# Optimization experiments

Measured on AMD Instinct MI355X. Metric: run time of the kernel, lower is better.

## Reference

```python
import jax, jax.numpy as jnp
import numpy as np
import math

B, S, E, NH = 1024, 16, 32, 4  # batch, seq, attn embed dim, heads
H = 64                          # lstm1 hidden; lstm2 hidden = H//2 = E


def _pos_encoding(s, d):
    pos = jnp.arange(s, dtype=jnp.float32)[:, None]
    div = jnp.exp(jnp.arange(0, d, 2, dtype=jnp.float32) * (-math.log(10000.0) / d))
    pe = jnp.zeros((s, d), jnp.float32)
    pe = pe.at[:, 0::2].set(jnp.sin(pos * div))
    pe = pe.at[:, 1::2].set(jnp.cos(pos * div))
    return pe


def _lstm(x, wih, whh, bih, bhh):
    # x: [B,S,in]; PyTorch gate order i,f,g,o; h0=c0=0
    b = x.shape[0]
    h_dim = whh.shape[1]
    xg = jnp.einsum('bsi,gi->bsg', x, wih) + bih + bhh  # precompute input contribution

    def step(carry, xt):
        h, c = carry
        g = xt + h @ whh.T
        i, f, gg, o = jnp.split(g, 4, axis=-1)
        c = jax.nn.sigmoid(f) * c + jax.nn.sigmoid(i) * jnp.tanh(gg)
        h = jax.nn.sigmoid(o) * jnp.tanh(c)
        return (h, c), h

    h0 = jnp.zeros((b, h_dim), x.dtype)
    _, hs = jax.lax.scan(step, (h0, h0), jnp.swapaxes(xg, 0, 1))
    return jnp.swapaxes(hs, 0, 1)  # [B,S,H]


def setup_inputs() -> dict:
    key = jax.random.key(0)
    ks = jax.random.split(key, 24)

    def rn(k, shape, s=0.15):
        return jax.random.normal(k, shape, jnp.float32) * s

    return {
        'x': jax.random.normal(ks[0], (B, S, 1), jnp.float32),
        'emb_w': rn(ks[1], (32, 1)), 'emb_b': rn(ks[2], (32,), 0.05),
        'l1_wih': rn(ks[3], (4 * H, 32)), 'l1_whh': rn(ks[4], (4 * H, H)),
        'l1_bih': rn(ks[5], (4 * H,), 0.05), 'l1_bhh': rn(ks[6], (4 * H,), 0.05),
        'l2_wih': rn(ks[7], (4 * (H // 2), H)), 'l2_whh': rn(ks[8], (4 * (H // 2), H // 2)),
        'l2_bih': rn(ks[9], (4 * (H // 2),), 0.05), 'l2_bhh': rn(ks[10], (4 * (H // 2),), 0.05),
        'attn_w': rn(ks[11], (3 * E, E)), 'attn_b': rn(ks[12], (3 * E,), 0.05),
        'attn_ow': rn(ks[13], (E, E)), 'attn_ob': rn(ks[14], (E,), 0.05),
        'd1_w': rn(ks[15], (64, E)), 'd1_b': rn(ks[16], (64,), 0.05),
        'bn1_g': jnp.ones((64,), jnp.float32), 'bn1_b': jnp.zeros((64,), jnp.float32),
        'd2_w': rn(ks[17], (32, 64)), 'd2_b': rn(ks[18], (32,), 0.05),
        'bn2_g': jnp.ones((32,), jnp.float32), 'bn2_b': jnp.zeros((32,), jnp.float32),
        'd3_w': rn(ks[19], (1, 32)), 'd3_b': rn(ks[20], (1,), 0.05),
    }


def reference(x, emb_w, emb_b, l1_wih, l1_whh, l1_bih, l1_bhh,
              l2_wih, l2_whh, l2_bih, l2_bhh,
              attn_w, attn_b, attn_ow, attn_ob,
              d1_w, d1_b, bn1_g, bn1_b, d2_w, d2_b, bn2_g, bn2_b, d3_w, d3_b):
    eps = 1e-5
    h = x @ emb_w.T + emb_b                      # [B,S,32]
    h = h + _pos_encoding(h.shape[1], h.shape[2])
    l1 = _lstm(h, l1_wih, l1_whh, l1_bih, l1_bhh)          # [B,S,64]  (dropout: eval -> id)
    l2 = _lstm(l1, l2_wih, l2_whh, l2_bih, l2_bhh)         # [B,S,32]
    l2 = l2 + l1[:, :, :l2.shape[2]]                        # residual

    # nn.MultiheadAttention with default batch_first=False: attends over axis 0 (=B here),
    # faithful to the original module's behavior.
    L, N, _ = l2.shape
    hd = E // NH
    qkv = l2 @ attn_w.T + attn_b
    q, k, v = jnp.split(qkv, 3, axis=-1)
    q = q.reshape(L, N, NH, hd) * (1.0 / math.sqrt(hd))
    k = k.reshape(L, N, NH, hd)
    v = v.reshape(L, N, NH, hd)
    scores = jnp.einsum('lnhd,mnhd->nhlm', q, k)           # [S,4,B,B]
    a = jax.nn.softmax(scores, axis=-1)
    att = jnp.einsum('nhlm,mnhd->lnhd', a, v).reshape(L, N, E)
    att = att @ attn_ow.T + attn_ob

    z = att[:, -1, :]                                       # [B,32]

    def bn(t, g, b):  # eval-mode BatchNorm1d with fresh running stats (mean=0, var=1)
        return t * (g / jnp.sqrt(1.0 + eps)) + b

    z = jax.nn.relu(bn(z @ d1_w.T + d1_b, bn1_g, bn1_b))
    z = jax.nn.relu(bn(z @ d2_w.T + d2_b, bn2_g, bn2_b))
    return jax.nn.sigmoid(z @ d3_w.T + d3_b)                # [B,1]
```

## Files before the change

### kernel.cpp

```cpp
#include <hip/hip_runtime.h>
#include <math.h>


__device__ __forceinline__ float sigf(float x) { return 1.0f / (1.0f + __expf(-x)); }
__device__ __forceinline__ float tanh_f(float x) {
    float a = fabsf(x);
    float e = __expf(2.0f * a);
    float t = 1.0f - 2.0f / (e + 1.0f);
    return copysignf(t, x);
}

__global__ void prep_kernel(const float* __restrict__ emb_w, const float* __restrict__ emb_b,
                            const float* __restrict__ wih1, const float* __restrict__ bih1,
                            const float* __restrict__ bhh1,
                            float* __restrict__ A1, float* __restrict__ C1) {
    int s = blockIdx.x, t = threadIdx.x;
    float c = bih1[t] + bhh1[t];
#pragma unroll
    for (int i = 0; i < 32; i++) {
        int j = (i >> 1) * 2;
        float div = __expf(-0.28782313662425574f * (float)j);
        float ang = (float)s * div;
        float pe = (i & 1) ? __cosf(ang) : __sinf(ang);
        c += (emb_b[i] + pe) * wih1[t * 32 + i];
    }
    C1[s * 256 + t] = c;
    if (s == 0) {
        float a = 0.f;
#pragma unroll
        for (int i = 0; i < 32; i++) a += emb_w[i] * wih1[t * 32 + i];
        A1[t] = a;
    }
}

__global__ __launch_bounds__(256, 2) void lstm_kernel(
    const float* __restrict__ x,
    const float* __restrict__ whh1,
    const float* __restrict__ wih2,
    const float* __restrict__ whh2,
    const float* __restrict__ bih2, const float* __restrict__ bhh2,
    const float* __restrict__ attn_w, const float* __restrict__ attn_b,
    const float* __restrict__ A1, const float* __restrict__ C1,
    float* __restrict__ Q, float* __restrict__ K, float* __restrict__ V) {
    int t = threadIdx.x;
    int base = blockIdx.x * 2;
    __shared__ __align__(16) float h1s[2][2][64];
    __shared__ __align__(16) float h2s[2][2][32];
    __shared__ __align__(16) float g1s[2][256];
    __shared__ __align__(16) float g2p[2][2][128];
    __shared__ __align__(16) float l2l[2][32];
    __shared__ float xs[2][16];

    float w1[64];
#pragma unroll
    for (int k = 0; k < 64; k++) w1[k] = whh1[t * 64 + k];
    int g = t & 127, half = t >> 7;
    float w2a[32];
#pragma unroll
    for (int k = 0; k < 32; k++) w2a[k] = wih2[g * 64 + half * 32 + k];
    float w2b[16];
#pragma unroll
    for (int k = 0; k < 16; k++) w2b[k] = whh2[g * 32 + half * 16 + k];
    float A1t = A1[t];
    float C1r[16];
#pragma unroll
    for (int s = 0; s < 16; s++) C1r[s] = C1[s * 256 + t];
    int j2 = t & 31;
    float bi2 = bih2[j2] + bhh2[j2];
    float bf2 = bih2[32 + j2] + bhh2[32 + j2];
    float bg2 = bih2[64 + j2] + bhh2[64 + j2];
    float bo2 = bih2[96 + j2] + bhh2[96 + j2];

    if (t < 128) h1s[0][t >> 6][t & 63] = 0.f;
    if (t < 64) h2s[0][t >> 5][t & 31] = 0.f;
    if (t < 32) xs[t >> 4][t & 15] = x[(base + (t >> 4)) * 16 + (t & 15)];
    float c1 = 0.f, c2 = 0.f;
    __syncthreads();

#pragma unroll
    for (int s = 0; s < 16; s++) {
        const int p = s & 1, pn = p ^ 1;
        {
            const float4* h0 = (const float4*)h1s[p][0];
            const float4* h1 = (const float4*)h1s[p][1];
            float a0 = xs[0][s] * A1t + C1r[s];
            float a1 = xs[1][s] * A1t + C1r[s];
#pragma unroll
            for (int k4 = 0; k4 < 16; k4++) {
                float4 u = h0[k4];
                float4 v = h1[k4];
                a0 += u.x * w1[4 * k4] + u.y * w1[4 * k4 + 1] + u.z * w1[4 * k4 + 2] + u.w * w1[4 * k4 + 3];
                a1 += v.x * w1[4 * k4] + v.y * w1[4 * k4 + 1] + v.z * w1[4 * k4 + 2] + v.w * w1[4 * k4 + 3];
            }
            g1s[0][t] = a0;
            g1s[1][t] = a1;
        }
        __syncthreads();
        if (t < 128) {
            int b = t >> 6, j = t & 63;
            float gi = g1s[b][j], gf = g1s[b][64 + j], gg = g1s[b][128 + j], go = g1s[b][192 + j];
            c1 = sigf(gf) * c1 + sigf(gi) * tanh_f(gg);
            h1s[pn][b][j] = sigf(go) * tanh_f(c1);
        }
        __syncthreads();
        {
#pragma unroll
            for (int b = 0; b < 2; b++) {
                const float4* hn = (const float4*)(&h1s[pn][b][half * 32]);
                const float4* ho = (const float4*)(&h2s[p][b][half * 16]);
                float d0 = 0.f, d1 = 0.f;
#pragma unroll
                for (int k4 = 0; k4 < 8; k4++) {
                    float4 u = hn[k4];
                    d0 += u.x * w2a[4 * k4] + u.y * w2a[4 * k4 + 1] + u.z * w2a[4 * k4 + 2] + u.w * w2a[4 * k4 + 3];
                }
#pragma unroll
                for (int k4 = 0; k4 < 4; k4++) {
                    float4 u = ho[k4];
                    d1 += u.x * w2b[4 * k4] + u.y * w2b[4 * k4 + 1] + u.z * w2b[4 * k4 + 2] + u.w * w2b[4 * k4 + 3];
                }
                g2p[b][half][g] = d0 + d1;
            }
        }
        __syncthreads();
        if (t < 64) {
            int b = t >> 5, j = t & 31;
            float gi = g2p[b][0][j] + g2p[b][1][j] + bi2;
            float gf = g2p[b][0][32 + j] + g2p[b][1][32 + j] + bf2;
            float gg = g2p[b][0][64 + j] + g2p[b][1][64 + j] + bg2;
            float go = g2p[b][0][96 + j] + g2p[b][1][96 + j] + bo2;
            c2 = sigf(gf) * c2 + sigf(gi) * tanh_f(gg);
            h2s[pn][b][j] = sigf(go) * tanh_f(c2);
        }
    }

    __syncthreads();
    if (t < 64) {
        int b = t >> 5, j = t & 31;
        l2l[b][j] = h2s[0][b][j] + h1s[0][b][j];
    }
    __syncthreads();
    if (t < 192) {
        int b = (t >= 96), r = t - b * 96;
        const float4* lw = (const float4*)l2l[b];
        const float4* aw = (const float4*)(attn_w + r * 32);
        float acc = attn_b[r];
#pragma unroll
        for (int k4 = 0; k4 < 8; k4++) {
            float4 u = lw[k4], w = aw[k4];
            acc += u.x * w.x + u.y * w.y + u.z * w.z + u.w * w.w;
        }
        int gb = base + b;
        if (r < 32) Q[gb * 32 + r] = acc * 0.35355339059327373f;
        else if (r < 64) K[gb * 32 + (r - 32)] = acc;
        else V[gb * 32 + (r - 64)] = acc;
    }
}

__global__ __launch_bounds__(256, 2) void attn_kernel(
    const float* __restrict__ Q, const float* __restrict__ K, const float* __restrict__ V,
    float* __restrict__ pm, float* __restrict__ ps, float* __restrict__ pacc) {
    int c = blockIdx.x & 15, lt = blockIdx.x >> 4;
    int t = threadIdx.x;
    int h = t >> 6, l = lt * 64 + (t & 63);
    __shared__ __align__(16) float Ks[64 * 32];
    __shared__ __align__(16) float Vs[64 * 32];
    {
        const float4* Kg = (const float4*)(K + c * 2048);
        const float4* Vg = (const float4*)(V + c * 2048);
        float4* K4 = (float4*)Ks;
        float4* V4 = (float4*)Vs;
        K4[t] = Kg[t];
        K4[t + 256] = Kg[t + 256];
        V4[t] = Vg[t];
        V4[t + 256] = Vg[t + 256];
    }
    const float4* qg = (const float4*)(Q + l * 32 + h * 8);
    float4 q0 = qg[0], q1 = qg[1];
    __syncthreads();
    float m_r = -1e30f, l_r = 0.f;
    float4 acc0 = {0, 0, 0, 0}, acc1 = {0, 0, 0, 0};
#pragma unroll 4
    for (int m = 0; m < 64; m++) {
        const float4* k4 = (const float4*)(Ks + m * 32 + h * 8);
        float4 ka = k4[0], kb = k4[1];
        float s = q0.x * ka.x + q0.y * ka.y + q0.z * ka.z + q0.w * ka.w +
                  q1.x * kb.x + q1.y * kb.y + q1.z * kb.z + q1.w * kb.w;
        const float4* v4 = (const float4*)(Vs + m * 32 + h * 8);
        float4 va = v4[0], vb = v4[1];
        float nm = fmaxf(m_r, s);
        float f = __expf(m_r - nm);
        float pp = __expf(s - nm);
        l_r = l_r * f + pp;
        acc0.x = acc0.x * f + pp * va.x;
        acc0.y = acc0.y * f + pp * va.y;
        acc0.z = acc0.z * f + pp * va.z;
        acc0.w = acc0.w * f + pp * va.w;
        acc1.x = acc1.x * f + pp * vb.x;
        acc1.y = acc1.y * f + pp * vb.y;
        acc1.z = acc1.z * f + pp * vb.z;
        acc1.w = acc1.w * f + pp * vb.w;
        m_r = nm;
    }
    int idx = (c * 4 + h) * 1024 + l;
    pm[idx] = m_r;
    ps[idx] = l_r;
    float4* po = (float4*)(pacc + idx * 8);
    po[0] = acc0;
    po[1] = acc1;
}

__global__ __launch_bounds__(256) void head_kernel(
    const float* __restrict__ pm, const float* __restrict__ ps, const float* __restrict__ pacc,
    const float* __restrict__ ow, const float* __restrict__ ob,
    const float* __restrict__ d1w, const float* __restrict__ d1b,
    const float* __restrict__ g1, const float* __restrict__ b1,
    const float* __restrict__ d2w, const float* __restrict__ d2b,
    const float* __restrict__ g2, const float* __restrict__ b2,
    const float* __restrict__ d3w, const float* __restrict__ d3b,
    float* __restrict__ out) {
    int wid = threadIdx.x >> 6, j = threadIdx.x & 63;
    int l = blockIdx.x * 4 + wid;
    __shared__ float att_s[4][32], z_s[4][32], r1s[4][64];
    if (j < 32) {
        int h = j >> 3, d = j & 7;
        float M = -1e30f;
#pragma unroll
        for (int c = 0; c < 16; c++) M = fmaxf(M, pm[(c * 4 + h) * 1024 + l]);
        float den = 0.f, num = 0.f;
#pragma unroll
        for (int c = 0; c < 16; c++) {
            int idx = (c * 4 + h) * 1024 + l;
            float e = __expf(pm[idx] - M);
            den += e * ps[idx];
            num += e * pacc[idx * 8 + d];
        }
        att_s[wid][j] = num / den;
    }
    __syncthreads();
    if (j < 32) {
        float a = ob[j];
#pragma unroll
        for (int i = 0; i < 32; i++) a += att_s[wid][i] * ow[j * 32 + i];
        z_s[wid][j] = a;
    }
    __syncthreads();
    const float inv = rsqrtf(1.0f + 1e-5f);
    if (j < 64) {
        float a = d1b[j];
#pragma unroll
        for (int i = 0; i < 32; i++) a += z_s[wid][i] * d1w[j * 32 + i];
        a = a * (g1[j] * inv) + b1[j];
        r1s[wid][j] = fmaxf(a, 0.f);
    }
    __syncthreads();
    if (j < 32) {
        float a = d2b[j];
#pragma unroll
        for (int i = 0; i < 64; i++) a += r1s[wid][i] * d2w[j * 64 + i];
        a = a * (g2[j] * inv) + b2[j];
        float r2 = fmaxf(a, 0.f);
        float p = r2 * d3w[j];
        p += __shfl_down(p, 16);
        p += __shfl_down(p, 8);
        p += __shfl_down(p, 4);
        p += __shfl_down(p, 2);
        p += __shfl_down(p, 1);
        if (j == 0) out[l] = 1.0f / (1.0f + __expf(-(p + d3b[0])));
    }
}

extern "C" void kernel_launch(void* const* d_in, const int* in_sizes, int n_in,
                              void* d_out, int out_size, void* d_ws, size_t ws_size,
                              hipStream_t stream) {
    const float* x      = (const float*)d_in[0];
    const float* emb_w  = (const float*)d_in[1];
    const float* emb_b  = (const float*)d_in[2];
    const float* l1_wih = (const float*)d_in[3];
    const float* l1_whh = (const float*)d_in[4];
    const float* l1_bih = (const float*)d_in[5];
    const float* l1_bhh = (const float*)d_in[6];
    const float* l2_wih = (const float*)d_in[7];
    const float* l2_whh = (const float*)d_in[8];
    const float* l2_bih = (const float*)d_in[9];
    const float* l2_bhh = (const float*)d_in[10];
    const float* attn_w = (const float*)d_in[11];
    const float* attn_b = (const float*)d_in[12];
    const float* attn_ow = (const float*)d_in[13];
    const float* attn_ob = (const float*)d_in[14];
    const float* d1_w  = (const float*)d_in[15];
    const float* d1_b  = (const float*)d_in[16];
    const float* bn1_g = (const float*)d_in[17];
    const float* bn1_b = (const float*)d_in[18];
    const float* d2_w  = (const float*)d_in[19];
    const float* d2_b  = (const float*)d_in[20];
    const float* bn2_g = (const float*)d_in[21];
    const float* bn2_b = (const float*)d_in[22];
    const float* d3_w  = (const float*)d_in[23];
    const float* d3_b  = (const float*)d_in[24];
    float* out = (float*)d_out;

    float* ws   = (float*)d_ws;
    float* A1   = ws;
    float* C1   = ws + 256;
    float* Q    = ws + 4352;
    float* K    = ws + 37120;
    float* V    = ws + 69888;
    float* pm   = ws + 102656;
    float* ps   = ws + 168192;
    float* pacc = ws + 233728;

    prep_kernel<<<16, 256, 0, stream>>>(emb_w, emb_b, l1_wih, l1_bih, l1_bhh, A1, C1);
    lstm_kernel<<<512, 256, 0, stream>>>(x, l1_whh, l2_wih, l2_whh, l2_bih, l2_bhh,
                                         attn_w, attn_b, A1, C1, Q, K, V);
    attn_kernel<<<256, 256, 0, stream>>>(Q, K, V, pm, ps, pacc);
    head_kernel<<<256, 256, 0, stream>>>(pm, ps, pacc, attn_ow, attn_ob, d1_w, d1_b,
                                         bn1_g, bn1_b, d2_w, d2_b, bn2_g, bn2_b,
                                         d3_w, d3_b, out);
}
```

Baseline: 159.6 us.

## Run both LSTM recurrences on bf16 MFMA with 16 sequences per block

The LSTM kernel now processes 16 batch rows per block with bf16 16x16x32 MFMA instructions, replacing the per-thread fp32 dot products. Weights are packed into registers as bf16 fragments, and hidden states go to XOR-swizzled LDS. The embedding plus positional-encoding input projection is folded into the MFMA as an extra K-slice, which removes the separate prep kernel. The grid drops from 512 to 64 blocks, trading parallelism for far fewer instructions per step, and bf16 rounding of weights and states adds precision risk.

```diff
diff --git a/kernel.cpp b/kernel.cpp
--- a/kernel.cpp
+++ b/kernel.cpp
@@ -1,6 +1,9 @@
 #include <hip/hip_runtime.h>
 #include <math.h>
 
+
+typedef __attribute__((ext_vector_type(8))) short short8v;
+typedef __attribute__((ext_vector_type(4))) float f32x4;
 
 __device__ __forceinline__ float sigf(float x) { return 1.0f / (1.0f + __expf(-x)); }
 __device__ __forceinline__ float tanh_f(float x) {
@@ -9,151 +12,210 @@
     float t = 1.0f - 2.0f / (e + 1.0f);
     return copysignf(t, x);
 }
-
-__global__ void prep_kernel(const float* __restrict__ emb_w, const float* __restrict__ emb_b,
-                            const float* __restrict__ wih1, const float* __restrict__ bih1,
-                            const float* __restrict__ bhh1,
-                            float* __restrict__ A1, float* __restrict__ C1) {
-    int s = blockIdx.x, t = threadIdx.x;
-    float c = bih1[t] + bhh1[t];
-#pragma unroll
-    for (int i = 0; i < 32; i++) {
-        int j = (i >> 1) * 2;
-        float div = __expf(-0.28782313662425574f * (float)j);
-        float ang = (float)s * div;
-        float pe = (i & 1) ? __cosf(ang) : __sinf(ang);
-        c += (emb_b[i] + pe) * wih1[t * 32 + i];
-    }
-    C1[s * 256 + t] = c;
-    if (s == 0) {
-        float a = 0.f;
-#pragma unroll
-        for (int i = 0; i < 32; i++) a += emb_w[i] * wih1[t * 32 + i];
-        A1[t] = a;
-    }
-}
-
-__global__ __launch_bounds__(256, 2) void lstm_kernel(
+__device__ __forceinline__ unsigned short f2bf(float f) {
+    unsigned int u = __float_as_uint(f);
+    unsigned int r = (u + 0x7FFFu + ((u >> 16) & 1u)) >> 16;
+    return (unsigned short)r;
+}
+
+__global__ __launch_bounds__(256, 1) void lstm_kernel(
     const float* __restrict__ x,
-    const float* __restrict__ whh1,
-    const float* __restrict__ wih2,
-    const float* __restrict__ whh2,
+    const float* __restrict__ emb_w, const float* __restrict__ emb_b,
+    const float* __restrict__ wih1, const float* __restrict__ whh1,
+    const float* __restrict__ bih1, const float* __restrict__ bhh1,
+    const float* __restrict__ wih2, const float* __restrict__ whh2,
     const float* __restrict__ bih2, const float* __restrict__ bhh2,
     const float* __restrict__ attn_w, const float* __restrict__ attn_b,
-    const float* __restrict__ A1, const float* __restrict__ C1,
     float* __restrict__ Q, float* __restrict__ K, float* __restrict__ V) {
-    int t = threadIdx.x;
-    int base = blockIdx.x * 2;
-    __shared__ __align__(16) float h1s[2][2][64];
-    __shared__ __align__(16) float h2s[2][2][32];
-    __shared__ __align__(16) float g1s[2][256];
-    __shared__ __align__(16) float g2p[2][2][128];
-    __shared__ __align__(16) float l2l[2][32];
-    __shared__ float xs[2][16];
-
-    float w1[64];
-#pragma unroll
-    for (int k = 0; k < 64; k++) w1[k] = whh1[t * 64 + k];
-    int g = t & 127, half = t >> 7;
-    float w2a[32];
-#pragma unroll
-    for (int k = 0; k < 32; k++) w2a[k] = wih2[g * 64 + half * 32 + k];
-    float w2b[16];
-#pragma unroll
-    for (int k = 0; k < 16; k++) w2b[k] = whh2[g * 32 + half * 16 + k];
-    float A1t = A1[t];
-    float C1r[16];
-#pragma unroll
-    for (int s = 0; s < 16; s++) C1r[s] = C1[s * 256 + t];
-    int j2 = t & 31;
-    float bi2 = bih2[j2] + bhh2[j2];
-    float bf2 = bih2[32 + j2] + bhh2[32 + j2];
-    float bg2 = bih2[64 + j2] + bhh2[64 + j2];
-    float bo2 = bih2[96 + j2] + bhh2[96 + j2];
-
-    if (t < 128) h1s[0][t >> 6][t & 63] = 0.f;
-    if (t < 64) h2s[0][t >> 5][t & 31] = 0.f;
-    if (t < 32) xs[t >> 4][t & 15] = x[(base + (t >> 4)) * 16 + (t & 15)];
-    float c1 = 0.f, c2 = 0.f;
-    __syncthreads();
+    const int tid = threadIdx.x;
+    const int w = tid >> 6, lane = tid & 63;
+    const int l15 = lane & 15, q4 = lane >> 4;
+    const int base = blockIdx.x * 16;
+
+    __shared__ __align__(16) unsigned char E_raw[16 * 1024];
+    __shared__ __align__(16) unsigned char H1_raw[2][2048];
+    __shared__ __align__(16) unsigned char H2_raw[2][1024];
+    __shared__ __align__(16) float L1F[16][64];
+    __shared__ __align__(16) float L2F[16][32];
+
+    const unsigned jx7 = (unsigned)(l15 & 7) << 4;
+    const unsigned jx4 = (unsigned)(l15 & 3) << 4;
+
+    short8v w1f[4][3];
+#pragma unroll
+    for (int t = 0; t < 4; t++) {
+        const int row = (w + 4 * t) * 16 + l15;
+#pragma unroll
+        for (int sl = 0; sl < 3; sl++) {
+            short8v f;
+#pragma unroll
+            for (int e = 0; e < 8; e++) {
+                int k = sl * 32 + q4 * 8 + e;
+                float v = (k < 64) ? whh1[row * 64 + k] : wih1[row * 32 + (k - 64)];
+                f[e] = (short)f2bf(v);
+            }
+            w1f[t][sl] = f;
+        }
+    }
+    float b1r[4][4];
+#pragma unroll
+    for (int t = 0; t < 4; t++)
+#pragma unroll
+        for (int e = 0; e < 4; e++) {
+            int r = (w + 4 * t) * 16 + q4 * 4 + e;
+            b1r[t][e] = bih1[r] + bhh1[r];
+        }
+
+    short8v w2f[4][3];
+    float b2r[4][4];
+    if (w < 2) {
+#pragma unroll
+        for (int t = 0; t < 4; t++) {
+            const int row = (w + 2 * t) * 16 + l15;
+#pragma unroll
+            for (int sl = 0; sl < 3; sl++) {
+                short8v f;
+#pragma unroll
+                for (int e = 0; e < 8; e++) {
+                    int k = sl * 32 + q4 * 8 + e;
+                    float v = (k < 64) ? wih2[row * 64 + k] : whh2[row * 32 + (k - 64)];
+                    f[e] = (short)f2bf(v);
+                }
+                w2f[t][sl] = f;
+            }
+#pragma unroll
+            for (int e = 0; e < 4; e++) {
+                int r = (w + 2 * t) * 16 + q4 * 4 + e;
+                b2r[t][e] = bih2[r] + bhh2[r];
+            }
+        }
+    }
+
+    *(unsigned long long*)(H1_raw[0] + tid * 8) = 0ULL;
+    if (tid < 128) *(unsigned long long*)(H2_raw[0] + tid * 8) = 0ULL;
+    {
+        const int je = tid >> 4, se = tid & 15;
+        float xv = x[(base + je) * 16 + se];
+        float ev[32];
+#pragma unroll
+        for (int ii = 0; ii < 16; ii++) {
+            float d = __expf(-0.28782313662425574f * (float)(2 * ii));
+            float ang = (float)se * d;
+            ev[2 * ii] = xv * emb_w[2 * ii] + emb_b[2 * ii] + __sinf(ang);
+            ev[2 * ii + 1] = xv * emb_w[2 * ii + 1] + emb_b[2 * ii + 1] + __cosf(ang);
+        }
+        unsigned jm = (unsigned)(je & 3) << 4;
+#pragma unroll
+        for (int b = 0; b < 4; b++) {
+            short8v pk;
+#pragma unroll
+            for (int e = 0; e < 8; e++) pk[e] = (short)f2bf(ev[b * 8 + e]);
+            *(short8v*)(&E_raw[se * 1024 + je * 64 + (((unsigned)(b * 16)) ^ jm)]) = pk;
+        }
+    }
+    float c1[4] = {0.f, 0.f, 0.f, 0.f};
+    float c2[4] = {0.f, 0.f, 0.f, 0.f};
+    __syncthreads();
+
+    const int u0 = w * 16 + q4 * 4;
+    const int u20 = w * 16 + q4 * 4;
 
 #pragma unroll
     for (int s = 0; s < 16; s++) {
         const int p = s & 1, pn = p ^ 1;
+        const unsigned char* H1p = H1_raw[p];
+        unsigned char* H1n = H1_raw[pn];
+        short8v B0 = *(const short8v*)(H1p + (((unsigned)(l15 * 128 + q4 * 16)) ^ jx7));
+        short8v B1 = *(const short8v*)(H1p + (((unsigned)(l15 * 128 + 64 + q4 * 16)) ^ jx7));
+        short8v BE = *(const short8v*)(&E_raw[s * 1024] + (((unsigned)(l15 * 64 + q4 * 16)) ^ jx4));
+        f32x4 a0 = {b1r[0][0], b1r[0][1], b1r[0][2], b1r[0][3]};
+        f32x4 a1 = {b1r[1][0], b1r[1][1], b1r[1][2], b1r[1][3]};
+        f32x4 a2 = {b1r[2][0], b1r[2][1], b1r[2][2], b1r[2][3]};
+        f32x4 a3 = {b1r[3][0], b1r[3][1], b1r[3][2], b1r[3][3]};
+        a0 = __builtin_amdgcn_mfma_f32_16x16x32_bf16(w1f[0][0], B0, a0, 0, 0, 0);
+        a1 = __builtin_amdgcn_mfma_f32_16x16x32_bf16(w1f[1][0], B0, a1, 0, 0, 0);
+        a2 = __builtin_amdgcn_mfma_f32_16x16x32_bf16(w1f[2][0], B0, a2, 0, 0, 0);
+        a3 = __builtin_amdgcn_mfma_f32_16x16x32_bf16(w1f[3][0], B0, a3, 0, 0, 0);
+        a0 = __builtin_amdgcn_mfma_f32_16x16x32_bf16(w1f[0][1], B1, a0, 0, 0, 0);
+        a1 = __builtin_amdgcn_mfma_f32_16x16x32_bf16(w1f[1][1], B1, a1, 0, 0, 0);
+        a2 = __builtin_amdgcn_mfma_f32_16x16x32_bf16(w1f[2][1], B1, a2, 0, 0, 0);
+        a3 = __builtin_amdgcn_mfma_f32_16x16x32_bf16(w1f[3][1], B1, a3, 0, 0, 0);
+        a0 = __builtin_amdgcn_mfma_f32_16x16x32_bf16(w1f[0][2], BE, a0, 0, 0, 0);
+        a1 = __builtin_amdgcn_mfma_f32_16x16x32_bf16(w1f[1][2], BE, a1, 0, 0, 0);
+        a2 = __builtin_amdgcn_mfma_f32_16x16x32_bf16(w1f[2][2], BE, a2, 0, 0, 0);
+        a3 = __builtin_amdgcn_mfma_f32_16x16x32_bf16(w1f[3][2], BE, a3, 0, 0, 0);
+        float h1v[4];
+#pragma unroll
+        for (int e = 0; e < 4; e++) {
+            c1[e] = sigf(a1[e]) * c1[e] + sigf(a0[e]) * tanh_f(a2[e]);
+            h1v[e] = sigf(a3[e]) * tanh_f(c1[e]);
+        }
         {
-            const float4* h0 = (const float4*)h1s[p][0];
-            const float4* h1 = (const float4*)h1s[p][1];
-            float a0 = xs[0][s] * A1t + C1r[s];
-            float a1 = xs[1][s] * A1t + C1r[s];
-#pragma unroll
-            for (int k4 = 0; k4 < 16; k4++) {
-                float4 u = h0[k4];
-                float4 v = h1[k4];
-                a0 += u.x * w1[4 * k4] + u.y * w1[4 * k4 + 1] + u.z * w1[4 * k4 + 2] + u.w * w1[4 * k4 + 3];
-                a1 += v.x * w1[4 * k4] + v.y * w1[4 * k4 + 1] + v.z * w1[4 * k4 + 2] + v.w * w1[4 * k4 + 3];
-            }
-            g1s[0][t] = a0;
-            g1s[1][t] = a1;
-        }
+            unsigned long long pk =
+                (unsigned long long)f2bf(h1v[0]) | ((unsigned long long)f2bf(h1v[1]) << 16) |
+                ((unsigned long long)f2bf(h1v[2]) << 32) | ((unsigned long long)f2bf(h1v[3]) << 48);
+            *(unsigned long long*)(H1n + (((unsigned)(l15 * 128 + u0 * 2)) ^ jx7)) = pk;
+        }
+        if (s == 15) *(float4*)(&L1F[l15][u0]) = make_float4(h1v[0], h1v[1], h1v[2], h1v[3]);
         __syncthreads();
-        if (t < 128) {
-            int b = t >> 6, j = t & 63;
-            float gi = g1s[b][j], gf = g1s[b][64 + j], gg = g1s[b][128 + j], go = g1s[b][192 + j];
-            c1 = sigf(gf) * c1 + sigf(gi) * tanh_f(gg);
-            h1s[pn][b][j] = sigf(go) * tanh_f(c1);
+        if (w < 2) {
+            const unsigned char* H2p = H2_raw[p];
+            short8v C0 = *(const short8v*)(H1n + (((unsigned)(l15 * 128 + q4 * 16)) ^ jx7));
+            short8v C1f = *(const short8v*)(H1n + (((unsigned)(l15 * 128 + 64 + q4 * 16)) ^ jx7));
+            short8v C2 = *(const short8v*)(H2p + (((unsigned)(l15 * 64 + q4 * 16)) ^ jx4));
+            f32x4 d0 = {b2r[0][0], b2r[0][1], b2r[0][2], b2r[0][3]};
+            f32x4 d1 = {b2r[1][0], b2r[1][1], b2r[1][2], b2r[1][3]};
+            f32x4 d2 = {b2r[2][0], b2r[2][1], b2r[2][2], b2r[2][3]};
+            f32x4 d3 = {b2r[3][0], b2r[3][1], b2r[3][2], b2r[3][3]};
+            d0 = __builtin_amdgcn_mfma_f32_16x16x32_bf16(w2f[0][0], C0, d0, 0, 0, 0);
+            d1 = __builtin_amdgcn_mfma_f32_16x16x32_bf16(w2f[1][0], C0, d1, 0, 0, 0);
+            d2 = __builtin_amdgcn_mfma_f32_16x16x32_bf16(w2f[2][0], C0, d2, 0, 0, 0);
+            d3 = __builtin_amdgcn_mfma_f32_16x16x32_bf16(w2f[3][0], C0, d3, 0, 0, 0);
+            d0 = __builtin_amdgcn_mfma_f32_16x16x32_bf16(w2f[0][1], C1f, d0, 0, 0, 0);
+            d1 = __builtin_amdgcn_mfma_f32_16x16x32_bf16(w2f[1][1], C1f, d1, 0, 0, 0);
+            d2 = __builtin_amdgcn_mfma_f32_16x16x32_bf16(w2f[2][1], C1f, d2, 0, 0, 0);
+            d3 = __builtin_amdgcn_mfma_f32_16x16x32_bf16(w2f[3][1], C1f, d3, 0, 0, 0);
+            d0 = __builtin_amdgcn_mfma_f32_16x16x32_bf16(w2f[0][2], C2, d0, 0, 0, 0);
+            d1 = __builtin_amdgcn_mfma_f32_16x16x32_bf16(w2f[1][2], C2, d1, 0, 0, 0);
+            d2 = __builtin_amdgcn_mfma_f32_16x16x32_bf16(w2f[2][2], C2, d2, 0, 0, 0);
+            d3 = __builtin_amdgcn_mfma_f32_16x16x32_bf16(w2f[3][2], C2, d3, 0, 0, 0);
+            float h2v[4];
+#pragma unroll
+            for (int e = 0; e < 4; e++) {
+                c2[e] = sigf(d1[e]) * c2[e] + sigf(d0[e]) * tanh_f(d2[e]);
+                h2v[e] = sigf(d3[e]) * tanh_f(c2[e]);
+            }
+            unsigned long long pk =
+                (unsigned long long)f2bf(h2v[0]) | ((unsigned long long)f2bf(h2v[1]) << 16) |
+                ((unsigned long long)f2bf(h2v[2]) << 32) | ((unsigned long long)f2bf(h2v[3]) << 48);
+            *(unsigned long long*)(H2_raw[pn] + (((unsigned)(l15 * 64 + u20 * 2)) ^ jx4)) = pk;
+            if (s == 15) *(float4*)(&L2F[l15][u20]) = make_float4(h2v[0], h2v[1], h2v[2], h2v[3]);
         }
         __syncthreads();
-        {
-#pragma unroll
-            for (int b = 0; b < 2; b++) {
-                const float4* hn = (const float4*)(&h1s[pn][b][half * 32]);
-                const float4* ho = (const float4*)(&h2s[p][b][half * 16]);
-                float d0 = 0.f, d1 = 0.f;
-#pragma unroll
-                for (int k4 = 0; k4 < 8; k4++) {
-                    float4 u = hn[k4];
-                    d0 += u.x * w2a[4 * k4] + u.y * w2a[4 * k4 + 1] + u.z * w2a[4 * k4 + 2] + u.w * w2a[4 * k4 + 3];
-                }
-#pragma unroll
-                for (int k4 = 0; k4 < 4; k4++) {
-                    float4 u = ho[k4];
-                    d1 += u.x * w2b[4 * k4] + u.y * w2b[4 * k4 + 1] + u.z * w2b[4 * k4 + 2] + u.w * w2b[4 * k4 + 3];
-                }
-                g2p[b][half][g] = d0 + d1;
-            }
-        }
-        __syncthreads();
-        if (t < 64) {
-            int b = t >> 5, j = t & 31;
-            float gi = g2p[b][0][j] + g2p[b][1][j] + bi2;
-            float gf = g2p[b][0][32 + j] + g2p[b][1][32 + j] + bf2;
-            float gg = g2p[b][0][64 + j] + g2p[b][1][64 + j] + bg2;
-            float go = g2p[b][0][96 + j] + g2p[b][1][96 + j] + bo2;
-            c2 = sigf(gf) * c2 + sigf(gi) * tanh_f(gg);
-            h2s[pn][b][j] = sigf(go) * tanh_f(c2);
-        }
-    }
-
-    __syncthreads();
-    if (t < 64) {
-        int b = t >> 5, j = t & 31;
-        l2l[b][j] = h2s[0][b][j] + h1s[0][b][j];
-    }
-    __syncthreads();
-    if (t < 192) {
-        int b = (t >= 96), r = t - b * 96;
-        const float4* lw = (const float4*)l2l[b];
-        const float4* aw = (const float4*)(attn_w + r * 32);
-        float acc = attn_b[r];
-#pragma unroll
-        for (int k4 = 0; k4 < 8; k4++) {
-            float4 u = lw[k4], w = aw[k4];
-            acc += u.x * w.x + u.y * w.y + u.z * w.z + u.w * w.w;
-        }
-        int gb = base + b;
-        if (r < 32) Q[gb * 32 + r] = acc * 0.35355339059327373f;
-        else if (r < 64) K[gb * 32 + (r - 32)] = acc;
-        else V[gb * 32 + (r - 64)] = acc;
+    }
+
+    {
+        const int j = tid >> 4, rb = tid & 15;
+        const int gb = base + j;
+        const float4* l1p = (const float4*)(&L1F[j][0]);
+        const float4* l2p = (const float4*)(&L2F[j][0]);
+#pragma unroll
+        for (int rep = 0; rep < 6; rep++) {
+            int row = rb + 16 * rep;
+            float acc = attn_b[row];
+            const float4* wrow = (const float4*)(attn_w + row * 32);
+#pragma unroll
+            for (int k4 = 0; k4 < 8; k4++) {
+                float4 lv1 = l1p[k4];
+                float4 lv2 = l2p[k4];
+                float4 ww = wrow[k4];
+                float lx = lv2.x + lv1.x, ly = lv2.y + lv1.y, lz = lv2.z + lv1.z, lw = lv2.w + lv1.w;
+                acc += lx * ww.x + ly * ww.y + lz * ww.z + lw * ww.w;
+            }
+            if (row < 32) Q[gb * 32 + row] = acc * 0.35355339059327373f;
+            else if (row < 64) K[gb * 32 + (row - 32)] = acc;
+            else V[gb * 32 + (row - 64)] = acc;
+        }
     }
 }
 
@@ -301,18 +363,16 @@
     float* out = (float*)d_out;
 
     float* ws   = (float*)d_ws;
-    float* A1   = ws;
-    float* C1   = ws + 256;
-    float* Q    = ws + 4352;
-    float* K    = ws + 37120;
-    float* V    = ws + 69888;
-    float* pm   = ws + 102656;
-    float* ps   = ws + 168192;
-    float* pacc = ws + 233728;
-
-    prep_kernel<<<16, 256, 0, stream>>>(emb_w, emb_b, l1_wih, l1_bih, l1_bhh, A1, C1);
-    lstm_kernel<<<512, 256, 0, stream>>>(x, l1_whh, l2_wih, l2_whh, l2_bih, l2_bhh,
-                                         attn_w, attn_b, A1, C1, Q, K, V);
+    float* Q    = ws;
+    float* K    = ws + 32768;
+    float* V    = ws + 65536;
+    float* pm   = ws + 98304;
+    float* ps   = ws + 163840;
+    float* pacc = ws + 229376;
+
+    lstm_kernel<<<64, 256, 0, stream>>>(x, emb_w, emb_b, l1_wih, l1_whh, l1_bih, l1_bhh,
+                                        l2_wih, l2_whh, l2_bih, l2_bhh,
+                                        attn_w, attn_b, Q, K, V);
     attn_kernel<<<256, 256, 0, stream>>>(Q, K, V, pm, ps, pacc);
     head_kernel<<<256, 256, 0, stream>>>(pm, ps, pacc, attn_ow, attn_ob, d1_w, d1_b,
                                          bn1_g, bn1_b, d2_w, d2_b, bn2_g, bn2_b,
```

New measurement: 166.8 us. 4.5% more time.
